# Optimization experiments

Hardware: AMD Instinct MI355X
Metric: run time of the kernel (lower is better)

Reference implementation:

```python
import jax, jax.numpy as jnp
import numpy as np

# Sampled softmax loss (tf.nn.sampled_softmax_loss with log-uniform candidate
# sampler, unique=True, remove_accidental_hits=True), vectorized over the batch
# instead of the original per-example tf.map_fn.

NEG_INF = -1e9


def _log_uniform_logp(ids, num_classes):
    # P(c) = (log(c+2) - log(c+1)) / log(num_classes + 1)
    ids = ids.astype(jnp.float32)
    return jnp.log(jnp.log1p(1.0 / (ids + 1.0)) / jnp.log(num_classes + 1.0))


def _log_expected_count(ids, num_sampled, num_classes):
    # unique sampling: E[count] = 1 - (1 - p)^num_sampled  (TF's formula)
    logp = _log_uniform_logp(ids, num_classes)
    return jnp.log(-jnp.expm1(num_sampled * jnp.log1p(-jnp.exp(logp))))


def setup_inputs() -> dict:
    key = jax.random.key(0)
    k1, k2, k3, k4 = jax.random.split(key, 4)
    B, T, D = 32, 512, 1024
    N, S = 50000, 4096
    x = jax.random.normal(k1, (B, T, D), dtype=jnp.float32)
    W = jax.random.normal(k2, (N, D), dtype=jnp.float32) * 0.02
    b = jnp.zeros((N,), dtype=jnp.float32)
    labels = jax.random.randint(k3, (B, T), 0, N, dtype=jnp.int64)
    sampled = jax.random.randint(k4, (B, S), 0, N, dtype=jnp.int64)
    return {"x": x, "W": W, "b": b, "labels": labels, "sampled": sampled}


def reference(x, W, b, labels, sampled):
    N = W.shape[0]
    S = sampled.shape[-1]
    # true class logits: [B,T]
    true_w = W[labels]                                   # [B,T,D] gather
    true_logit = jnp.einsum("btd,btd->bt", x, true_w) + b[labels]
    true_logit = true_logit - _log_expected_count(labels, S, N)
    # sampled class logits: [B,T,S]
    samp_w = W[sampled]                                  # [B,S,D] gather
    samp_logits = jnp.einsum("btd,bsd->bts", x, samp_w)
    samp_logits = samp_logits + (b[sampled] - _log_expected_count(sampled, S, N))[:, None, :]
    # remove accidental hits (sampled id == true label)
    hit = sampled[:, None, :] == labels[:, :, None]      # [B,T,S]
    samp_logits = jnp.where(hit, NEG_INF, samp_logits)
    # softmax cross-entropy with the true class at index 0
    all_logits = jnp.concatenate([true_logit[..., None], samp_logits], axis=-1)
    token_loss = jax.nn.logsumexp(all_logits, axis=-1) - true_logit  # [B,T]
    per_example = jnp.mean(token_loss, axis=-1)                      # [B]
    return 0.5 * jnp.mean(per_example)
```

## Files before the change

### kernel.cpp

```cpp
#include <hip/hip_runtime.h>
#include <hip/hip_bf16.h>
#include <math.h>
#include <stdint.h>

#define B_ 32
#define T_ 512
#define D_ 1024
#define N_ 50000
#define S_ 4096

#define INV_LOG_NP1 0.09242317f

#define WSCALE 64.0f
#define INV_WSCALE 0.015625f
#define LOG2E 1.4426950408889634f

typedef __attribute__((ext_vector_type(8))) short bf16x8;
typedef __attribute__((ext_vector_type(4))) float f32x4;
typedef __attribute__((ext_vector_type(4))) short s16x4;

__device__ __forceinline__ short f2bf(float f) {
    unsigned u = __float_as_uint(f);
    u += 0x7fffu + ((u >> 16) & 1u);
    return (short)(u >> 16);
}

__device__ __forceinline__ int pack_fp8x4(float a, float b, float c, float d) {
    int v = __builtin_amdgcn_cvt_pk_fp8_f32(a, b, 0, false);
    v = __builtin_amdgcn_cvt_pk_fp8_f32(c, d, v, true);
    return v;
}

__device__ __forceinline__ float log_expected(int id) {
    float p  = log1pf(1.0f / ((float)id + 1.0f)) * INV_LOG_NP1;
    return logf(-expm1f((float)S_ * log1pf(-p)));
}

__device__ __forceinline__ void gload_lds16(const void* g, void* l) {
    __builtin_amdgcn_global_load_lds(
        (const __attribute__((address_space(1))) void*)g,
        (__attribute__((address_space(3))) void*)l, 16, 0, 0);
}

__global__ __launch_bounds__(256) void prep_kernel(
    const float* __restrict__ x, const float* __restrict__ W,
    const float* __restrict__ bvec, const int* __restrict__ labels,
    float* __restrict__ true_logit, float* __restrict__ denom,
    unsigned char* __restrict__ xf8, unsigned char* __restrict__ Wf8)
{
    constexpr int NCVT = N_ * D_ / 2048;
    if (blockIdx.x < NCVT) {
        size_t i = ((size_t)blockIdx.x * 2048) + (size_t)threadIdx.x * 8;
        float4 a = *(const float4*)(W + i);
        float4 b = *(const float4*)(W + i + 4);
        int2 o;
        o.x = pack_fp8x4(a.x * WSCALE, a.y * WSCALE, a.z * WSCALE, a.w * WSCALE);
        o.y = pack_fp8x4(b.x * WSCALE, b.y * WSCALE, b.z * WSCALE, b.w * WSCALE);
        *(int2*)(Wf8 + i) = o;
        return;
    }
    int w = threadIdx.x >> 6, lane = threadIdx.x & 63;
    int token = (blockIdx.x - NCVT) * 4 + w;
    int lab = labels[token];
    const float4* xp = (const float4*)(x + (size_t)token * D_);
    const float4* wp = (const float4*)(W + (size_t)lab * D_);
    float acc = 0.0f;
#pragma unroll
    for (int j = 0; j < 4; ++j) {
        float4 a = xp[lane + 64 * j];
        float4 c = wp[lane + 64 * j];
        acc += a.x * c.x + a.y * c.y + a.z * c.z + a.w * c.w;
        int o = pack_fp8x4(a.x, a.y, a.z, a.w);
        *(int*)(xf8 + (size_t)token * D_ + (lane + 64 * j) * 4) = o;
    }
#pragma unroll
    for (int m = 32; m >= 1; m >>= 1) acc += __shfl_xor(acc, m);
    if (lane == 0) {
        float tl = acc + bvec[lab] - log_expected(lab);
        true_logit[token] = tl;
        denom[token] = __expf(tl);
    }
}

__global__ __launch_bounds__(256) void true_logit_kernel(
    const float* __restrict__ x, const float* __restrict__ W,
    const float* __restrict__ bvec, const int* __restrict__ labels,
    float* __restrict__ true_logit, float* __restrict__ denom)
{
    int w = threadIdx.x >> 6, lane = threadIdx.x & 63;
    int token = blockIdx.x * 4 + w;
    int lab = labels[token];
    const float4* xp = (const float4*)(x + (size_t)token * D_);
    const float4* wp = (const float4*)(W + (size_t)lab * D_);
    float acc = 0.0f;
#pragma unroll
    for (int j = 0; j < 4; ++j) {
        float4 a = xp[lane + 64 * j];
        float4 c = wp[lane + 64 * j];
        acc += a.x * c.x + a.y * c.y + a.z * c.z + a.w * c.w;
    }
#pragma unroll
    for (int m = 32; m >= 1; m >>= 1) acc += __shfl_xor(acc, m);
    if (lane == 0) {
        float tl = acc + bvec[lab] - log_expected(lab);
        true_logit[token] = tl;
        denom[token] = __expf(tl);
    }
}

constexpr int BM = 128, BN = 128;

__global__ __launch_bounds__(256) void sampled_gemm_fp8(
    const unsigned char* __restrict__ xf8, const unsigned char* __restrict__ Wf8,
    const float* __restrict__ bvec, const int* __restrict__ labels,
    const int* __restrict__ sampled, float* __restrict__ denom)
{
    constexpr int BK = 128;
    __shared__ __align__(16) unsigned char At[BM * BK];
    __shared__ __align__(16) unsigned char Bt[BN * BK];
    __shared__ float colbias[BN];
    __shared__ int   ids[BN];
    __shared__ int   labT[BM];

    int bidx = blockIdx.x;
    int b    = bidx >> 7;
    int rem  = bidx & 127;
    int mT   = rem >> 5;
    int nT   = rem & 31;

    int tid  = threadIdx.x;
    int w    = tid >> 6, lane = tid & 63;

    int r = lane >> 3;
    int s = lane & 7;
    int c = s ^ r;

    int tokBase = b * T_ + mT * BM;
    const unsigned char* gA[4];
    const unsigned char* gB[4];
    unsigned char* lA[4];
    unsigned char* lB[4];
#pragma unroll
    for (int j = 0; j < 4; ++j) {
        int seg = 4 * w + j;
        int row = seg * 8 + r;
        gA[j] = xf8 + (size_t)(tokBase + row) * D_ + c * 16;
        int id = sampled[b * S_ + nT * BN + row];
        gB[j] = Wf8 + (size_t)id * D_ + c * 16;
        lA[j] = At + seg * 1024;
        lB[j] = Bt + seg * 1024;
    }

#define STAGE()                                                      \
    do {                                                             \
        _Pragma("unroll")                                            \
        for (int j = 0; j < 4; ++j) { gload_lds16(gA[j], lA[j]); gA[j] += BK; } \
        _Pragma("unroll")                                            \
        for (int j = 0; j < 4; ++j) { gload_lds16(gB[j], lB[j]); gB[j] += BK; } \
    } while (0)

    STAGE();

    if (tid < BN) {
        int id = sampled[b * S_ + nT * BN + tid];
        ids[tid] = id;
        colbias[tid] = (bvec[id] - log_expected(id)) * LOG2E;
    } else {
        int i = tid - BN;
        labT[i] = labels[b * T_ + mT * BM + i];
    }

    f32x4 acc[4][4];
#pragma unroll
    for (int mi = 0; mi < 4; ++mi)
#pragma unroll
        for (int ni = 0; ni < 4; ++ni) acc[mi][ni] = (f32x4){0.f, 0.f, 0.f, 0.f};

    int waveM = w >> 1, waveN = w & 1;
    int lr = lane & 15, lq = lane >> 4;
    int aRow[4], bRow[4];
#pragma unroll
    for (int i = 0; i < 4; ++i) {
        aRow[i] = (waveM * 64 + i * 16 + lr) * BK;
        bRow[i] = (waveN * 64 + i * 16 + lr) * BK;
    }
    int offP[2];
#pragma unroll
    for (int tp = 0; tp < 2; ++tp)
        offP[tp] = ((2 * lq + tp) ^ (lr & 7)) * 16;

    for (int k0 = 0; k0 < D_; k0 += BK) {
        if (k0) {
            __syncthreads();
            STAGE();
        }
        __syncthreads();
#pragma unroll
        for (int tp = 0; tp < 2; ++tp) {
            long2 av[4], bv[4];
#pragma unroll
            for (int mi = 0; mi < 4; ++mi)
                av[mi] = *(const long2*)(At + aRow[mi] + offP[tp]);
#pragma unroll
            for (int ni = 0; ni < 4; ++ni)
                bv[ni] = *(const long2*)(Bt + bRow[ni] + offP[tp]);
#pragma unroll
            for (int mi = 0; mi < 4; ++mi)
#pragma unroll
                for (int ni = 0; ni < 4; ++ni)
                    acc[mi][ni] = __builtin_amdgcn_mfma_f32_16x16x32_fp8_fp8(
                        av[mi].x, bv[ni].x, acc[mi][ni], 0, 0, 0);
#pragma unroll
            for (int mi = 0; mi < 4; ++mi)
#pragma unroll
                for (int ni = 0; ni < 4; ++ni)
                    acc[mi][ni] = __builtin_amdgcn_mfma_f32_16x16x32_fp8_fp8(
                        av[mi].y, bv[ni].y, acc[mi][ni], 0, 0, 0);
        }
    }
#undef STAGE

    const float accScale = INV_WSCALE * LOG2E;
    float* dptr = denom + b * T_ + mT * BM;
#pragma unroll
    for (int mi = 0; mi < 4; ++mi) {
#pragma unroll
        for (int rr = 0; rr < 4; ++rr) {
            int localRow = waveM * 64 + mi * 16 + lq * 4 + rr;
            int lab = labT[localRow];
            float sum = 0.0f;
#pragma unroll
            for (int ni = 0; ni < 4; ++ni) {
                int col = waveN * 64 + ni * 16 + lr;
                float v = acc[mi][ni][rr] * accScale + colbias[col];
                sum += (ids[col] == lab) ? 0.0f : exp2f(v);
            }
            sum += __shfl_xor(sum, 1);
            sum += __shfl_xor(sum, 2);
            sum += __shfl_xor(sum, 4);
            sum += __shfl_xor(sum, 8);
            if (lr == 0) atomicAdd(&dptr[localRow], sum);
        }
    }
}

__global__ __launch_bounds__(256) void sampled_gemm(
    const float* __restrict__ x, const float* __restrict__ W,
    const float* __restrict__ bvec, const int* __restrict__ labels,
    const int* __restrict__ sampled, float* __restrict__ denom)
{
    constexpr int FBK = 32;
    __shared__ short At[BM * FBK];
    __shared__ short Bt[BN * FBK];
    __shared__ float colbias[BN];
    __shared__ int   ids[BN];
    __shared__ int   labT[BM];

    int bidx = blockIdx.x;
    int b    = bidx >> 7;
    int rem  = bidx & 127;
    int mT   = rem >> 5;
    int nT   = rem & 31;
    int tid = threadIdx.x;

    if (tid < BN) {
        int id = sampled[b * S_ + nT * BN + tid];
        ids[tid] = id;
        colbias[tid] = bvec[id] - log_expected(id);
    } else {
        int i = tid - BN;
        labT[i] = labels[b * T_ + mT * BM + i];
    }
    __syncthreads();

    const float* asrc[4];
    const float* bsrc[4];
    int ch = tid & 7;
#pragma unroll
    for (int j = 0; j < 4; ++j) {
        int row = (tid >> 3) + 32 * j;
        asrc[j] = x + ((size_t)(b * T_ + mT * BM + row)) * D_ + ch * 4;
        bsrc[j] = W + (size_t)ids[row] * D_ + ch * 4;
    }

    f32x4 acc[4][4];
#pragma unroll
    for (int mi = 0; mi < 4; ++mi)
#pragma unroll
        for (int ni = 0; ni < 4; ++ni) acc[mi][ni] = (f32x4){0.f, 0.f, 0.f, 0.f};

    int w = tid >> 6, lane = tid & 63;
    int waveM = w >> 1, waveN = w & 1;
    int lr = lane & 15, lq = lane >> 4;

    for (int k0 = 0; k0 < D_; k0 += FBK) {
        __syncthreads();
#pragma unroll
        for (int j = 0; j < 4; ++j) {
            int row = (tid >> 3) + 32 * j;
            float4 va = *(const float4*)(asrc[j] + k0);
            s16x4 pa = {f2bf(va.x), f2bf(va.y), f2bf(va.z), f2bf(va.w)};
            *(s16x4*)&At[row * FBK + ch * 4] = pa;
            float4 vb = *(const float4*)(bsrc[j] + k0);
            s16x4 pb = {f2bf(vb.x), f2bf(vb.y), f2bf(vb.z), f2bf(vb.w)};
            *(s16x4*)&Bt[row * FBK + ch * 4] = pb;
        }
        __syncthreads();
        bf16x8 af[4], bfr[4];
#pragma unroll
        for (int mi = 0; mi < 4; ++mi)
            af[mi] = *(const bf16x8*)&At[(waveM * 64 + mi * 16 + lr) * FBK + lq * 8];
#pragma unroll
        for (int ni = 0; ni < 4; ++ni)
            bfr[ni] = *(const bf16x8*)&Bt[(waveN * 64 + ni * 16 + lr) * FBK + lq * 8];
#pragma unroll
        for (int mi = 0; mi < 4; ++mi)
#pragma unroll
            for (int ni = 0; ni < 4; ++ni)
                acc[mi][ni] = __builtin_amdgcn_mfma_f32_16x16x32_bf16(
                    af[mi], bfr[ni], acc[mi][ni], 0, 0, 0);
    }

    float* dptr = denom + b * T_ + mT * BM;
#pragma unroll
    for (int mi = 0; mi < 4; ++mi) {
#pragma unroll
        for (int rr = 0; rr < 4; ++rr) {
            int localRow = waveM * 64 + mi * 16 + lq * 4 + rr;
            int lab = labT[localRow];
            float sum = 0.0f;
#pragma unroll
            for (int ni = 0; ni < 4; ++ni) {
                int col = waveN * 64 + ni * 16 + lr;
                float v = acc[mi][ni][rr] + colbias[col];
                sum += (ids[col] == lab) ? 0.0f : __expf(v);
            }
            sum += __shfl_xor(sum, 1);
            sum += __shfl_xor(sum, 2);
            sum += __shfl_xor(sum, 4);
            sum += __shfl_xor(sum, 8);
            if (lr == 0) atomicAdd(&dptr[localRow], sum);
        }
    }
}

__global__ __launch_bounds__(256) void finalize_kernel(
    const float* __restrict__ true_logit, const float* __restrict__ denom,
    float* __restrict__ out)
{
    float s = 0.0f;
    for (int i = threadIdx.x; i < B_ * T_; i += 256)
        s += __logf(denom[i]) - true_logit[i];
#pragma unroll
    for (int m = 32; m >= 1; m >>= 1) s += __shfl_xor(s, m);
    __shared__ float wsum[4];
    if ((threadIdx.x & 63) == 0) wsum[threadIdx.x >> 6] = s;
    __syncthreads();
    if (threadIdx.x == 0)
        out[0] = 0.5f * (wsum[0] + wsum[1] + wsum[2] + wsum[3]) / (float)(B_ * T_);
}

extern "C" void kernel_launch(void* const* d_in, const int* in_sizes, int n_in,
                              void* d_out, int out_size, void* d_ws, size_t ws_size,
                              hipStream_t stream) {
    const float* x       = (const float*)d_in[0];
    const float* W       = (const float*)d_in[1];
    const float* bvec    = (const float*)d_in[2];
    const int*   labels  = (const int*)d_in[3];
    const int*   sampled = (const int*)d_in[4];
    float* out = (float*)d_out;

    float* true_logit   = (float*)d_ws;
    float* denom        = true_logit + B_ * T_;
    unsigned char* xf8  = (unsigned char*)(denom + B_ * T_);
    unsigned char* Wf8  = xf8 + (size_t)B_ * T_ * D_;

    const size_t NEED = (size_t)2 * B_ * T_ * 4
                      + (size_t)B_ * T_ * D_
                      + (size_t)N_ * D_;

    if (ws_size >= NEED) {
        prep_kernel<<<N_ * D_ / 2048 + B_ * T_ / 4, 256, 0, stream>>>(
            x, W, bvec, labels, true_logit, denom, xf8, Wf8);
        sampled_gemm_fp8<<<B_ * (T_ / BM) * (S_ / BN), 256, 0, stream>>>(
            xf8, Wf8, bvec, labels, sampled, denom);
    } else {
        true_logit_kernel<<<B_ * T_ / 4, 256, 0, stream>>>(
            x, W, bvec, labels, true_logit, denom);
        sampled_gemm<<<B_ * (T_ / BM) * (S_ / BN), 256, 0, stream>>>(
            x, W, bvec, labels, sampled, denom);
    }
    finalize_kernel<<<1, 256, 0, stream>>>(true_logit, denom, out);
}
```

Baseline: 485.2 us.

## Enlarge FP8 sampled GEMM tile to 256x256 with double-buffered LDS

Replaces the 128x128 FP8 GEMM block with a 256x256 tile run by 512 threads (8 waves). Each wave now computes 128x64 instead of 64x64. The LDS A/B buffers are double-buffered, and explicit waitcnt/barrier control lets the next K-slice load overlap the MFMA work on the current one. This improves operand reuse per global load and hides load latency. The cost is 128KB of LDS per block, higher register pressure from 32 accumulator tiles, and only 512 blocks in the grid.

```diff
diff --git a/kernel.cpp b/kernel.cpp
--- a/kernel.cpp
+++ b/kernel.cpp
@@ -108,25 +108,24 @@
     }
 }
 
-constexpr int BM = 128, BN = 128;
-
-__global__ __launch_bounds__(256) void sampled_gemm_fp8(
+__global__ __launch_bounds__(512, 2) void sampled_gemm_fp8_256(
     const unsigned char* __restrict__ xf8, const unsigned char* __restrict__ Wf8,
     const float* __restrict__ bvec, const int* __restrict__ labels,
     const int* __restrict__ sampled, float* __restrict__ denom)
 {
-    constexpr int BK = 128;
-    __shared__ __align__(16) unsigned char At[BM * BK];
-    __shared__ __align__(16) unsigned char Bt[BN * BK];
-    __shared__ float colbias[BN];
-    __shared__ int   ids[BN];
-    __shared__ int   labT[BM];
+    constexpr int BM2 = 256, BN2 = 256, BK2 = 128;
+    constexpr int TILE = BM2 * BK2;
+    __shared__ __align__(16) unsigned char At[2][TILE];
+    __shared__ __align__(16) unsigned char Bt[2][TILE];
+    __shared__ float colbias[BN2];
+    __shared__ int   ids[BN2];
+    __shared__ int   labT[BM2];
 
     int bidx = blockIdx.x;
-    int b    = bidx >> 7;
-    int rem  = bidx & 127;
-    int mT   = rem >> 5;
-    int nT   = rem & 31;
+    int b    = bidx >> 5;
+    int rem  = bidx & 31;
+    int mT   = rem >> 4;
+    int nT   = rem & 15;
 
     int tid  = threadIdx.x;
     int w    = tid >> 6, lane = tid & 63;
@@ -135,98 +134,106 @@
     int s = lane & 7;
     int c = s ^ r;
 
-    int tokBase = b * T_ + mT * BM;
+    int tokBase = b * T_ + mT * BM2;
     const unsigned char* gA[4];
     const unsigned char* gB[4];
-    unsigned char* lA[4];
-    unsigned char* lB[4];
+    int lOff[4];
 #pragma unroll
     for (int j = 0; j < 4; ++j) {
         int seg = 4 * w + j;
         int row = seg * 8 + r;
         gA[j] = xf8 + (size_t)(tokBase + row) * D_ + c * 16;
-        int id = sampled[b * S_ + nT * BN + row];
+        int id = sampled[b * S_ + nT * BN2 + row];
         gB[j] = Wf8 + (size_t)id * D_ + c * 16;
-        lA[j] = At + seg * 1024;
-        lB[j] = Bt + seg * 1024;
-    }
-
-#define STAGE()                                                      \
-    do {                                                             \
-        _Pragma("unroll")                                            \
-        for (int j = 0; j < 4; ++j) { gload_lds16(gA[j], lA[j]); gA[j] += BK; } \
-        _Pragma("unroll")                                            \
-        for (int j = 0; j < 4; ++j) { gload_lds16(gB[j], lB[j]); gB[j] += BK; } \
+        lOff[j] = seg * 1024;
+    }
+
+#define STAGE(buf)                                                            \
+    do {                                                                      \
+        _Pragma("unroll")                                                     \
+        for (int j = 0; j < 4; ++j) { gload_lds16(gA[j], At[buf] + lOff[j]); gA[j] += BK2; } \
+        _Pragma("unroll")                                                     \
+        for (int j = 0; j < 4; ++j) { gload_lds16(gB[j], Bt[buf] + lOff[j]); gB[j] += BK2; } \
     } while (0)
 
-    STAGE();
-
-    if (tid < BN) {
-        int id = sampled[b * S_ + nT * BN + tid];
+    STAGE(0);
+    if (tid < BN2) {
+        int id = sampled[b * S_ + nT * BN2 + tid];
         ids[tid] = id;
         colbias[tid] = (bvec[id] - log_expected(id)) * LOG2E;
     } else {
-        int i = tid - BN;
-        labT[i] = labels[b * T_ + mT * BM + i];
-    }
-
-    f32x4 acc[4][4];
-#pragma unroll
-    for (int mi = 0; mi < 4; ++mi)
+        int i = tid - BN2;
+        labT[i] = labels[b * T_ + mT * BM2 + i];
+    }
+    STAGE(1);
+    asm volatile("s_waitcnt vmcnt(8) lgkmcnt(0)" ::: "memory");
+    __builtin_amdgcn_sched_barrier(0);
+    __builtin_amdgcn_s_barrier();
+    asm volatile("" ::: "memory");
+
+    f32x4 acc[8][4];
+#pragma unroll
+    for (int mi = 0; mi < 8; ++mi)
 #pragma unroll
         for (int ni = 0; ni < 4; ++ni) acc[mi][ni] = (f32x4){0.f, 0.f, 0.f, 0.f};
 
-    int waveM = w >> 1, waveN = w & 1;
+    int waveM = w >> 2, waveN = w & 3;
     int lr = lane & 15, lq = lane >> 4;
-    int aRow[4], bRow[4];
-#pragma unroll
-    for (int i = 0; i < 4; ++i) {
-        aRow[i] = (waveM * 64 + i * 16 + lr) * BK;
-        bRow[i] = (waveN * 64 + i * 16 + lr) * BK;
-    }
+    int aRow[8], bRow[4];
+#pragma unroll
+    for (int i = 0; i < 8; ++i) aRow[i] = (waveM * 128 + i * 16 + lr) * BK2;
+#pragma unroll
+    for (int i = 0; i < 4; ++i) bRow[i] = (waveN * 64 + i * 16 + lr) * BK2;
     int offP[2];
 #pragma unroll
     for (int tp = 0; tp < 2; ++tp)
         offP[tp] = ((2 * lq + tp) ^ (lr & 7)) * 16;
 
-    for (int k0 = 0; k0 < D_; k0 += BK) {
-        if (k0) {
-            __syncthreads();
-            STAGE();
-        }
-        __syncthreads();
+    for (int t = 0; t < 8; ++t) {
+        const unsigned char* Ac = At[t & 1];
+        const unsigned char* Bc = Bt[t & 1];
 #pragma unroll
         for (int tp = 0; tp < 2; ++tp) {
-            long2 av[4], bv[4];
-#pragma unroll
-            for (int mi = 0; mi < 4; ++mi)
-                av[mi] = *(const long2*)(At + aRow[mi] + offP[tp]);
+            long2 bv[4];
 #pragma unroll
             for (int ni = 0; ni < 4; ++ni)
-                bv[ni] = *(const long2*)(Bt + bRow[ni] + offP[tp]);
-#pragma unroll
-            for (int mi = 0; mi < 4; ++mi)
+                bv[ni] = *(const long2*)(Bc + bRow[ni] + offP[tp]);
+#pragma unroll
+            for (int mi = 0; mi < 8; ++mi) {
+                long2 av = *(const long2*)(Ac + aRow[mi] + offP[tp]);
 #pragma unroll
                 for (int ni = 0; ni < 4; ++ni)
                     acc[mi][ni] = __builtin_amdgcn_mfma_f32_16x16x32_fp8_fp8(
-                        av[mi].x, bv[ni].x, acc[mi][ni], 0, 0, 0);
-#pragma unroll
-            for (int mi = 0; mi < 4; ++mi)
+                        av.x, bv[ni].x, acc[mi][ni], 0, 0, 0);
 #pragma unroll
                 for (int ni = 0; ni < 4; ++ni)
                     acc[mi][ni] = __builtin_amdgcn_mfma_f32_16x16x32_fp8_fp8(
-                        av[mi].y, bv[ni].y, acc[mi][ni], 0, 0, 0);
+                        av.y, bv[ni].y, acc[mi][ni], 0, 0, 0);
+            }
         }
+        if (t == 7) break;
+        asm volatile("" ::: "memory");
+        __builtin_amdgcn_s_barrier();
+        asm volatile("" ::: "memory");
+        if (t < 6) {
+            STAGE(t & 1);
+            asm volatile("s_waitcnt vmcnt(8)" ::: "memory");
+        } else {
+            asm volatile("s_waitcnt vmcnt(0)" ::: "memory");
+        }
+        __builtin_amdgcn_sched_barrier(0);
+        __builtin_amdgcn_s_barrier();
+        asm volatile("" ::: "memory");
     }
 #undef STAGE
 
     const float accScale = INV_WSCALE * LOG2E;
-    float* dptr = denom + b * T_ + mT * BM;
-#pragma unroll
-    for (int mi = 0; mi < 4; ++mi) {
+    float* dptr = denom + b * T_ + mT * BM2;
+#pragma unroll
+    for (int mi = 0; mi < 8; ++mi) {
 #pragma unroll
         for (int rr = 0; rr < 4; ++rr) {
-            int localRow = waveM * 64 + mi * 16 + lq * 4 + rr;
+            int localRow = waveM * 128 + mi * 16 + lq * 4 + rr;
             int lab = labT[localRow];
             float sum = 0.0f;
 #pragma unroll
@@ -244,6 +251,8 @@
     }
 }
 
+constexpr int BM = 128, BN = 128;
+
 __global__ __launch_bounds__(256) void sampled_gemm(
     const float* __restrict__ x, const float* __restrict__ W,
     const float* __restrict__ bvec, const int* __restrict__ labels,
@@ -382,7 +391,7 @@
     if (ws_size >= NEED) {
         prep_kernel<<<N_ * D_ / 2048 + B_ * T_ / 4, 256, 0, stream>>>(
             x, W, bvec, labels, true_logit, denom, xf8, Wf8);
-        sampled_gemm_fp8<<<B_ * (T_ / BM) * (S_ / BN), 256, 0, stream>>>(
+        sampled_gemm_fp8_256<<<B_ * (T_ / 256) * (S_ / 256), 512, 0, stream>>>(
             xf8, Wf8, bvec, labels, sampled, denom);
     } else {
         true_logit_kernel<<<B_ * T_ / 4, 256, 0, stream>>>(
```

After: 514.1 us. 1.06x slower.
